# Kernel tuning notes

Hardware: AMD Instinct MI355X
Metric: run time of the kernel (lower is better)

## Reference

```python
import jax, jax.numpy as jnp
import numpy as np
from jax import lax

LOG2PI = float(np.log(2.0 * np.pi))
N_K, N_T, N_C, N_D, N_SPK = 256, 128, 32, 10, 1000000

def _std_normal_logpdf(x):
    return -0.5 * (x * x + LOG2PI)

def _normal_logpdf(x, mu, log_sig):
    z = (x - mu) * jnp.exp(-log_sig)
    return -0.5 * (z * z + LOG2PI) - log_sig

def safe_log(x, minval=1e-10):
    return jnp.log(x + minval)

def setup_inputs() -> dict:
    key = jax.random.key(0)
    ks_ = jax.random.split(key, 8)
    s = jax.random.normal(ks_[0], (N_SPK, N_D), dtype=jnp.float32)
    y = jax.random.normal(ks_[1], (N_K, N_T), dtype=jnp.float32)
    ks = jax.random.randint(ks_[2], (N_SPK,), 0, N_K, dtype=jnp.int32)
    ts = jax.random.randint(ks_[3], (N_SPK,), 0, N_T, dtype=jnp.int32)
    means = jax.random.normal(ks_[4], (N_C, N_D), dtype=jnp.float32)
    A = jax.random.normal(ks_[5], (N_C, N_D, N_D), dtype=jnp.float32)
    covs = jnp.einsum('cij,ckj->cik', A, A) / N_D + jnp.eye(N_D, dtype=jnp.float32)
    b_mu = jax.random.normal(ks_[6], (N_C,), dtype=jnp.float32)
    b_log_sig = jax.random.normal(ks_[7], (N_C,), dtype=jnp.float32)
    beta_mu = jax.random.normal(jax.random.fold_in(key, 10), (N_C, N_T), dtype=jnp.float32)
    beta_log_sig = jax.random.normal(jax.random.fold_in(key, 11), (N_C, N_T), dtype=jnp.float32)
    return {"s": s, "y": y, "ks": ks, "ts": ts, "means": means, "covs": covs,
            "b_mu": b_mu, "b_log_sig": b_log_sig, "beta_mu": beta_mu, "beta_log_sig": beta_log_sig}

def _mvn_ll(s, means, covs):
    # ll[n, c] = MVN(means[c], covs[c]).log_prob(s[n]); loop over small n_c via lax.map
    L = jnp.linalg.cholesky(covs)                       # (c, d, d)
    logdet = 2.0 * jnp.sum(jnp.log(jnp.diagonal(L, axis1=1, axis2=2)), axis=1)  # (c,)
    d = s.shape[1]
    def comp(args):
        mu, Lc, ld = args
        diff = s - mu                                   # (n, d)
        z = jax.scipy.linalg.solve_triangular(Lc, diff.T, lower=True)  # (d, n)
        return -0.5 * (d * LOG2PI + ld + jnp.sum(z * z, axis=0))       # (n,)
    return lax.map(comp, (means, L, logdet)).T          # (n, c)

def reference(s, y, ks, ts, means, covs, b_mu, b_log_sig, beta_mu, beta_log_sig):
    # sampling=False path: use variational means
    b_sample, beta_sample = b_mu, beta_mu               # (c,), (c, t)
    # log_lambdas[k, c, t] = b[c] + beta[c, t] * y[k, t]
    log_lambdas = b_sample[None, :, None] + beta_sample[None, :, :] * y[:, None, :]
    log_pis = jax.nn.log_softmax(log_lambdas, axis=1)   # (k, c, t)
    ll = _mvn_ll(s, means, covs)                        # (n, c)
    logits = ll + log_pis[ks, :, ts]                    # per-spike gather -> (n, c)
    r = jax.nn.softmax(logits, axis=1)                  # responsibilities (n, c)
    log_prior = jnp.sum(_std_normal_logpdf(b_sample)) + jnp.sum(_std_normal_logpdf(beta_sample))
    log_q = jnp.sum(_normal_logpdf(b_sample, b_mu, b_log_sig)) + \
            jnp.sum(_normal_logpdf(beta_sample, beta_mu, beta_log_sig))
    elbo = log_prior - log_q
    elbo += jnp.sum(r * logits)
    elbo -= jnp.sum(r * safe_log(r))
    return elbo
```

## Files before the change

### kernel.cpp

```cpp
#include <hip/hip_runtime.h>
#include <hip/hip_bf16.h>
#include <hip/hip_fp16.h>
#include <math.h>

#define NK 256
#define NT 128
#define NC 32
#define ND 10
#define NSPK 1000000
#define LOG2PI 1.8378770664093453f
#define NCHUNK ((NSPK + 255) / 256)
#define GRID 1024

#define FSTR 36
#define LDS_DW (256 * FSTR)

typedef __attribute__((ext_vector_type(8))) short short8;
typedef __attribute__((ext_vector_type(4))) float floatx4;
typedef __attribute__((ext_vector_type(4))) int intx4;

union FragCvt { intx4 i; short8 s; };
union H2Cvt { int i; __half2 h; };


__device__ inline unsigned pack_bf16(float a, float b) {
  __hip_bfloat16 ha = __float2bfloat16(a), hb = __float2bfloat16(b);
  unsigned short ua, ub;
  __builtin_memcpy(&ua, &ha, 2);
  __builtin_memcpy(&ub, &hb, 2);
  return (unsigned)ua | ((unsigned)ub << 16);
}

__global__ void prep_kernel(const float* __restrict__ y,
                            const float* __restrict__ means,
                            const float* __restrict__ covs,
                            const float* __restrict__ b_mu,
                            const float* __restrict__ b_ls,
                            const float* __restrict__ beta_mu,
                            const float* __restrict__ beta_ls,
                            int* __restrict__ wt,
                            float* __restrict__ cpack,
                            __half* __restrict__ pisT,
                            double* __restrict__ acc,
                            unsigned int* __restrict__ counter,
                            unsigned int* __restrict__ queue) {
  int blk = blockIdx.x;
  int tid = threadIdx.x;

  if (blk == 0) {
    int c = tid;
    if (c >= NC) return;

    float M[ND][ND];
    #pragma unroll
    for (int i = 0; i < ND; ++i)
      #pragma unroll
      for (int j = 0; j < ND; ++j)
        M[i][j] = covs[c * ND * ND + i * ND + j];

    float logdet = 0.f;
    #pragma unroll
    for (int j = 0; j < ND; ++j) {
      float d = M[j][j];
      #pragma unroll
      for (int k = 0; k < ND; ++k) if (k < j) d -= M[j][k] * M[j][k];
      float sq = sqrtf(d);
      M[j][j] = sq;
      logdet += 2.f * __logf(sq);
      float inv = 1.f / sq;
      #pragma unroll
      for (int i = 0; i < ND; ++i) {
        if (i > j) {
          float s2 = M[i][j];
          #pragma unroll
          for (int k = 0; k < ND; ++k) if (k < j) s2 -= M[i][k] * M[j][k];
          M[i][j] = s2 * inv;
        }
      }
    }

    #pragma unroll
    for (int j = 0; j < ND; ++j) {
      M[j][j] = 1.f / M[j][j];
      #pragma unroll
      for (int i = 0; i < ND; ++i) {
        if (i > j) {
          float s2 = 0.f;
          #pragma unroll
          for (int k = 0; k < ND; ++k) if (k >= j && k < i) s2 += M[i][k] * M[k][j];
          M[i][j] = -s2 / M[i][i];
        }
      }
    }

    float pd[ND];
    #pragma unroll
    for (int i = 0; i < ND; ++i) {
      #pragma unroll
      for (int jj = 0; jj < ND; ++jj) {
        if (jj >= i) {
          float s2 = 0.f;
          #pragma unroll
          for (int k = 0; k < ND; ++k) if (k >= jj) s2 += M[k][i] * M[k][jj];
          if (jj > i) M[i][jj] = s2;
          else pd[i] = s2;
        }
      }
    }

    float mu[ND], q[ND];
    #pragma unroll
    for (int i = 0; i < ND; ++i) mu[i] = means[c * ND + i];
    float muPmu = 0.f;
    #pragma unroll
    for (int i = 0; i < ND; ++i) {
      float a2 = pd[i] * mu[i];
      #pragma unroll
      for (int j = 0; j < ND; ++j) {
        if (j < i) a2 += M[j][i] * mu[j];
        if (j > i) a2 += M[i][j] * mu[j];
      }
      q[i] = a2;
      muPmu += mu[i] * a2;
    }
    float cst = -0.5f * ((float)ND * LOG2PI + logdet + muPmu);

    float wv[64];
    int p = 0;
    #pragma unroll
    for (int i = 0; i < ND; ++i)
      #pragma unroll
      for (int j = 0; j < ND; ++j)
        if (j >= i && !(i == 9 && j == 9))
          wv[p++] = (i == j) ? -0.5f * pd[i] : -M[i][j];
    #pragma unroll
    for (int i = 0; i < ND; ++i) wv[54 + i] = q[i];

    #pragma unroll
    for (int j = 0; j < 32; ++j) {
      float a = wv[2 * j], b = wv[2 * j + 1];
      float ah = __bfloat162float(__float2bfloat16(a));
      float bh = __bfloat162float(__float2bfloat16(b));
      wt[c * 32 + j] = (int)pack_bf16(ah, bh);
      wt[(32 + c) * 32 + j] = (int)pack_bf16(a - ah, b - bh);
    }
    cpack[c] = cst;
    cpack[32 + c] = -0.5f * pd[9];

  } else if (blk == 1) {
    float local = 0.f;
    for (int i = tid; i < NC; i += 256)
      local += fmaf(-0.5f * b_mu[i], b_mu[i], b_ls[i]);
    for (int i = tid; i < NC * NT; i += 256)
      local += fmaf(-0.5f * beta_mu[i], beta_mu[i], beta_ls[i]);
    #pragma unroll
    for (int off = 32; off > 0; off >>= 1) local += __shfl_down(local, off);
    __shared__ float red[4];
    if ((tid & 63) == 0) red[tid >> 6] = local;
    __syncthreads();
    if (tid == 0) {
      acc[0] = (double)(red[0] + red[1] + red[2] + red[3]);
      counter[0] = 0u;
      queue[0] = GRID;
    }

  } else {
    int id = (blk - 2) * 256 + tid;
    int t = id & (NT - 1);
    float yv = y[id];
    float v[NC];
    float m = -1e30f;
    #pragma unroll
    for (int c = 0; c < NC; ++c) {
      v[c] = fmaf(beta_mu[c * NT + t], yv, b_mu[c]);
      m = fmaxf(m, v[c]);
    }
    float ssum = 0.f;
    #pragma unroll
    for (int c = 0; c < NC; ++c) ssum += __expf(v[c] - m);
    float lz = m + __logf(ssum);
    __half* outp = pisT + (size_t)id * NC;
    #pragma unroll
    for (int c = 0; c < NC; ++c) outp[c] = __float2half(v[c] - lz);
  }
}

__global__ void __launch_bounds__(256)
__attribute__((amdgpu_waves_per_eu(4, 4)))
spike_kernel(const float* __restrict__ s,
             const int* __restrict__ ks,
             const int* __restrict__ ts,
             const int* __restrict__ wt,
             const float* __restrict__ cpack,
             const __half* __restrict__ pisT,
             double* __restrict__ acc,
             unsigned int* __restrict__ counter,
             unsigned int* __restrict__ queue,
             float* __restrict__ out) {
  __shared__ int lds[LDS_DW];
  __shared__ float red[4];
  __shared__ int nextc_sh;

  int tid = threadIdx.x;
  int wv_ = tid >> 6, L = tid & 63;
  int r = L & 15, q = L >> 4;

  FragCvt bf[2][2][2];
  #pragma unroll
  for (int h = 0; h < 2; ++h)
    #pragma unroll
    for (int nt = 0; nt < 2; ++nt)
      #pragma unroll
      for (int ks2 = 0; ks2 < 2; ++ks2)
        bf[h][nt][ks2].i =
            *(const intx4*)&wt[(h * 32 + nt * 16 + r) * 32 + ks2 * 16 + q * 4];

  float lse_sum = 0.f;

  int chunk = blockIdx.x;
  float svc[ND];
  int ktc;
  {
    int n = chunk * 256 + tid;
    int nc = n < NSPK ? n : (NSPK - 1);
    const float2* srow = (const float2*)(s + (size_t)nc * ND);
    #pragma unroll
    for (int i = 0; i < 5; ++i) {
      float2 v2 = srow[i];
      svc[2 * i] = v2.x;
      svc[2 * i + 1] = v2.y;
    }
    ktc = ks[nc] * NT + ts[nc];
  }

  while (chunk < NCHUNK) {
    int ncur = chunk * 256 + tid;

    __syncthreads();

    {
      int rb = tid * FSTR;
      float f[8];
      int p = 0;
      #pragma unroll
      for (int i = 0; i < ND; ++i) {
        #pragma unroll
        for (int j = i; j < ND; ++j) {
          if (i == 9 && j == 9) continue;
          f[p & 7] = svc[i] * svc[j];
          if ((p & 7) == 7) {
            intx4 v;
            v.x = (int)pack_bf16(f[0], f[1]);
            v.y = (int)pack_bf16(f[2], f[3]);
            v.z = (int)pack_bf16(f[4], f[5]);
            v.w = (int)pack_bf16(f[6], f[7]);
            *(intx4*)&lds[rb + (p >> 3) * 4] = v;
          }
          ++p;
        }
      }
      #pragma unroll
      for (int i = 0; i < ND; ++i) {
        f[p & 7] = svc[i];
        if ((p & 7) == 7) {
          intx4 v;
          v.x = (int)pack_bf16(f[0], f[1]);
          v.y = (int)pack_bf16(f[2], f[3]);
          v.z = (int)pack_bf16(f[4], f[5]);
          v.w = (int)pack_bf16(f[6], f[7]);
          *(intx4*)&lds[rb + (p >> 3) * 4] = v;
        }
        ++p;
      }
    }

    if (tid == 0) nextc_sh = (int)atomicAdd(queue, 1u);

    __syncthreads();

    int nextc = nextc_sh;

    float svn[ND];
    int ktn;
    {
      int cc = nextc < NCHUNK ? nextc : (NCHUNK - 1);
      int n = cc * 256 + tid;
      int nc = n < NSPK ? n : (NSPK - 1);
      const float2* srow = (const float2*)(s + (size_t)nc * ND);
      #pragma unroll
      for (int i = 0; i < 5; ++i) {
        float2 v2 = srow[i];
        svn[2 * i] = v2.x;
        svn[2 * i + 1] = v2.y;
      }
      ktn = ks[nc] * NT + ts[nc];
    }

    floatx4 accf[4][2];
    #pragma unroll
    for (int mt = 0; mt < 4; ++mt)
      #pragma unroll
      for (int nt = 0; nt < 2; ++nt)
        accf[mt][nt] = (floatx4){0.f, 0.f, 0.f, 0.f};

    #pragma unroll
    for (int mt = 0; mt < 4; ++mt) {
      #pragma unroll
      for (int ks2 = 0; ks2 < 2; ++ks2) {
        FragCvt a;
        a.i = *(const intx4*)&lds[(wv_ * 64 + mt * 16 + r) * FSTR + ks2 * 16 + q * 4];
        #pragma unroll
        for (int nt = 0; nt < 2; ++nt) {
          accf[mt][nt] = __builtin_amdgcn_mfma_f32_16x16x32_bf16(
              a.s, bf[0][nt][ks2].s, accf[mt][nt], 0, 0, 0);
          accf[mt][nt] = __builtin_amdgcn_mfma_f32_16x16x32_bf16(
              a.s, bf[1][nt][ks2].s, accf[mt][nt], 0, 0, 0);
        }
      }
    }

    __syncthreads();

    #pragma unroll
    for (int mt = 0; mt < 4; ++mt)
      #pragma unroll
      for (int nt = 0; nt < 2; ++nt)
        #pragma unroll
        for (int rr = 0; rr < 4; ++rr) {
          int srow_ = wv_ * 64 + mt * 16 + q * 4 + rr;
          lds[srow_ * FSTR + nt * 16 + r] = __float_as_int(accf[mt][nt][rr]);
        }
    __syncthreads();

    {
      const intx4* lpp = (const intx4*)(pisT + (size_t)ktc * NC);
      intx4 lraw[4];
      #pragma unroll
      for (int i = 0; i < 4; ++i) lraw[i] = lpp[i];

      float s9sq = svc[9] * svc[9];
      int base = tid * FSTR;
      float lg[32];
      #pragma unroll
      for (int g = 0; g < 8; ++g) {
        intx4 lv = *(const intx4*)&lds[base + g * 4];
        lg[4 * g + 0] = __int_as_float(lv.x);
        lg[4 * g + 1] = __int_as_float(lv.y);
        lg[4 * g + 2] = __int_as_float(lv.z);
        lg[4 * g + 3] = __int_as_float(lv.w);
      }
      #pragma unroll
      for (int g = 0; g < 16; ++g) {
        H2Cvt hc;
        hc.i = ((const int*)lraw)[g];
        float lo = __low2float(hc.h), hi = __high2float(hc.h);
        lg[2 * g + 0] += lo + fmaf(cpack[32 + 2 * g + 0], s9sq, cpack[2 * g + 0]);
        lg[2 * g + 1] += hi + fmaf(cpack[32 + 2 * g + 1], s9sq, cpack[2 * g + 1]);
      }

      float m = lg[0];
      #pragma unroll
      for (int c = 1; c < 32; ++c) m = fmaxf(m, lg[c]);
      float ssum = 0.f;
      #pragma unroll
      for (int c = 0; c < 32; ++c) ssum += __expf(lg[c] - m);
      if (ncur < NSPK) lse_sum += m + __logf(ssum);
    }

    chunk = nextc;
    ktc = ktn;
    #pragma unroll
    for (int i = 0; i < ND; ++i) svc[i] = svn[i];
  }

  #pragma unroll
  for (int off = 32; off > 0; off >>= 1) lse_sum += __shfl_down(lse_sum, off);
  if ((tid & 63) == 0) red[tid >> 6] = lse_sum;
  __syncthreads();
  if (tid == 0) {
    atomicAdd(acc, (double)(red[0] + red[1] + red[2] + red[3]));
    __threadfence();
    unsigned int old = atomicAdd(counter, 1u);
    if (old == GRID - 1) {
      __threadfence();
      double v = atomicAdd(acc, 0.0);
      out[0] = (float)v;
    }
  }
}

extern "C" void kernel_launch(void* const* d_in, const int* in_sizes, int n_in,
                              void* d_out, int out_size, void* d_ws, size_t ws_size,
                              hipStream_t stream) {
  const float* s       = (const float*)d_in[0];
  const float* y       = (const float*)d_in[1];
  const int*   ks      = (const int*)d_in[2];
  const int*   ts      = (const int*)d_in[3];
  const float* means   = (const float*)d_in[4];
  const float* covs    = (const float*)d_in[5];
  const float* b_mu    = (const float*)d_in[6];
  const float* b_ls    = (const float*)d_in[7];
  const float* beta_mu = (const float*)d_in[8];
  const float* beta_ls = (const float*)d_in[9];
  float* out = (float*)d_out;

  char* ws = (char*)d_ws;
  double* acc           = (double*)ws;
  unsigned int* counter = (unsigned int*)(ws + 8);
  unsigned int* queue   = (unsigned int*)(ws + 12);
  float* cpack          = (float*)(ws + 64);
  int* wt               = (int*)(ws + 1024);
  __half* pisT          = (__half*)(ws + 16384);

  prep_kernel<<<2 + (NK * NT) / 256, 256, 0, stream>>>(
      y, means, covs, b_mu, b_ls, beta_mu, beta_ls, wt, cpack, pisT, acc,
      counter, queue);
  spike_kernel<<<GRID, 256, 0, stream>>>(
      s, ks, ts, wt, cpack, pisT, acc, counter, queue, out);
}
```

Measured before the change: 169.0 us.

## Make spike kernel wave-independent with static scheduling and per-wave LDS

Each wave now processes its own 64-spike chunk with a private LDS slice, which removes the block-wide __syncthreads and the atomic work queue in favor of a static grid-stride over waves. The MFMA roles are swapped so the weights are the A operand and spike features the B operand, letting results be written back as float4 rows. The per-cluster constant is folded into the gathered log-pi table by a separate prep kernel, which adds a kernel launch. The pisT gather is issued earlier to hide its latency. Static scheduling can cause load imbalance, and NSPK/64 divides evenly, so no tail guard is needed.

```diff
diff --git a/kernel.cpp b/kernel.cpp
--- a/kernel.cpp
+++ b/kernel.cpp
@@ -9,11 +9,10 @@
 #define ND 10
 #define NSPK 1000000
 #define LOG2PI 1.8378770664093453f
-#define NCHUNK ((NSPK + 255) / 256)
+#define NWCHUNK (NSPK / 64)
 #define GRID 1024
-
-#define FSTR 36
-#define LDS_DW (256 * FSTR)
+#define NWAVES (GRID * 4)
+#define LSTR 33
 
 typedef __attribute__((ext_vector_type(8))) short short8;
 typedef __attribute__((ext_vector_type(4))) float floatx4;
@@ -31,19 +30,16 @@
   return (unsigned)ua | ((unsigned)ub << 16);
 }
 
-__global__ void prep_kernel(const float* __restrict__ y,
-                            const float* __restrict__ means,
-                            const float* __restrict__ covs,
-                            const float* __restrict__ b_mu,
-                            const float* __restrict__ b_ls,
-                            const float* __restrict__ beta_mu,
-                            const float* __restrict__ beta_ls,
-                            int* __restrict__ wt,
-                            float* __restrict__ cpack,
-                            __half* __restrict__ pisT,
-                            double* __restrict__ acc,
-                            unsigned int* __restrict__ counter,
-                            unsigned int* __restrict__ queue) {
+__global__ void prep1_kernel(const float* __restrict__ means,
+                             const float* __restrict__ covs,
+                             const float* __restrict__ b_mu,
+                             const float* __restrict__ b_ls,
+                             const float* __restrict__ beta_mu,
+                             const float* __restrict__ beta_ls,
+                             int* __restrict__ wt,
+                             float* __restrict__ cpack,
+                             double* __restrict__ acc,
+                             unsigned int* __restrict__ counter) {
   int blk = blockIdx.x;
   int tid = threadIdx.x;
 
@@ -108,7 +104,7 @@
       }
     }
 
-    float mu[ND], q[ND];
+    float mu[ND], qv[ND];
     #pragma unroll
     for (int i = 0; i < ND; ++i) mu[i] = means[c * ND + i];
     float muPmu = 0.f;
@@ -120,7 +116,7 @@
         if (j < i) a2 += M[j][i] * mu[j];
         if (j > i) a2 += M[i][j] * mu[j];
       }
-      q[i] = a2;
+      qv[i] = a2;
       muPmu += mu[i] * a2;
     }
     float cst = -0.5f * ((float)ND * LOG2PI + logdet + muPmu);
@@ -134,7 +130,7 @@
         if (j >= i && !(i == 9 && j == 9))
           wv[p++] = (i == j) ? -0.5f * pd[i] : -M[i][j];
     #pragma unroll
-    for (int i = 0; i < ND; ++i) wv[54 + i] = q[i];
+    for (int i = 0; i < ND; ++i) wv[54 + i] = qv[i];
 
     #pragma unroll
     for (int j = 0; j < 32; ++j) {
@@ -147,7 +143,7 @@
     cpack[c] = cst;
     cpack[32 + c] = -0.5f * pd[9];
 
-  } else if (blk == 1) {
+  } else {
     float local = 0.f;
     for (int i = tid; i < NC; i += 256)
       local += fmaf(-0.5f * b_mu[i], b_mu[i], b_ls[i]);
@@ -161,28 +157,32 @@
     if (tid == 0) {
       acc[0] = (double)(red[0] + red[1] + red[2] + red[3]);
       counter[0] = 0u;
-      queue[0] = GRID;
-    }
-
-  } else {
-    int id = (blk - 2) * 256 + tid;
-    int t = id & (NT - 1);
-    float yv = y[id];
-    float v[NC];
-    float m = -1e30f;
-    #pragma unroll
-    for (int c = 0; c < NC; ++c) {
-      v[c] = fmaf(beta_mu[c * NT + t], yv, b_mu[c]);
-      m = fmaxf(m, v[c]);
-    }
-    float ssum = 0.f;
-    #pragma unroll
-    for (int c = 0; c < NC; ++c) ssum += __expf(v[c] - m);
-    float lz = m + __logf(ssum);
-    __half* outp = pisT + (size_t)id * NC;
-    #pragma unroll
-    for (int c = 0; c < NC; ++c) outp[c] = __float2half(v[c] - lz);
+    }
   }
+}
+
+__global__ void prep2_kernel(const float* __restrict__ y,
+                             const float* __restrict__ b_mu,
+                             const float* __restrict__ beta_mu,
+                             const float* __restrict__ cpack,
+                             __half* __restrict__ pisT) {
+  int id = blockIdx.x * 256 + threadIdx.x;
+  int t = id & (NT - 1);
+  float yv = y[id];
+  float v[NC];
+  float m = -1e30f;
+  #pragma unroll
+  for (int c = 0; c < NC; ++c) {
+    v[c] = fmaf(beta_mu[c * NT + t], yv, b_mu[c]);
+    m = fmaxf(m, v[c]);
+  }
+  float ssum = 0.f;
+  #pragma unroll
+  for (int c = 0; c < NC; ++c) ssum += __expf(v[c] - m);
+  float lz = m + __logf(ssum);
+  __half* outp = pisT + (size_t)id * NC;
+  #pragma unroll
+  for (int c = 0; c < NC; ++c) outp[c] = __float2half(v[c] - lz + cpack[c]);
 }
 
 __global__ void __launch_bounds__(256)
@@ -195,51 +195,57 @@
              const __half* __restrict__ pisT,
              double* __restrict__ acc,
              unsigned int* __restrict__ counter,
-             unsigned int* __restrict__ queue,
              float* __restrict__ out) {
-  __shared__ int lds[LDS_DW];
+  __shared__ int lds[4 * 64 * LSTR];
   __shared__ float red[4];
-  __shared__ int nextc_sh;
 
   int tid = threadIdx.x;
-  int wv_ = tid >> 6, L = tid & 63;
+  int wid = tid >> 6, L = tid & 63;
   int r = L & 15, q = L >> 4;
-
-  FragCvt bf[2][2][2];
+  int* ldsw = &lds[wid * 64 * LSTR];
+
+  FragCvt wf[2][2][2];
   #pragma unroll
   for (int h = 0; h < 2; ++h)
     #pragma unroll
-    for (int nt = 0; nt < 2; ++nt)
-      #pragma unroll
-      for (int ks2 = 0; ks2 < 2; ++ks2)
-        bf[h][nt][ks2].i =
-            *(const intx4*)&wt[(h * 32 + nt * 16 + r) * 32 + ks2 * 16 + q * 4];
+    for (int mt = 0; mt < 2; ++mt)
+      #pragma unroll
+      for (int kk = 0; kk < 2; ++kk)
+        wf[h][mt][kk].i =
+            *(const intx4*)&wt[(h * 32 + mt * 16 + r) * 32 + kk * 16 + q * 4];
+
+  float w99v[NC];
+  #pragma unroll
+  for (int c = 0; c < NC; ++c) w99v[c] = cpack[32 + c];
 
   float lse_sum = 0.f;
-
-  int chunk = blockIdx.x;
+  int g = blockIdx.x * 4 + wid;
+
+  int c = g;
   float svc[ND];
-  int ktc;
+  int kvc, tvc;
   {
-    int n = chunk * 256 + tid;
-    int nc = n < NSPK ? n : (NSPK - 1);
-    const float2* srow = (const float2*)(s + (size_t)nc * ND);
+    int n = c * 64 + L;
+    const float2* srow = (const float2*)(s + (size_t)n * ND);
     #pragma unroll
     for (int i = 0; i < 5; ++i) {
       float2 v2 = srow[i];
       svc[2 * i] = v2.x;
       svc[2 * i + 1] = v2.y;
     }
-    ktc = ks[nc] * NT + ts[nc];
+    kvc = ks[n];
+    tvc = ts[n];
   }
 
-  while (chunk < NCHUNK) {
-    int ncur = chunk * 256 + tid;
-
-    __syncthreads();
+  while (c < NWCHUNK) {
+    int ktc = kvc * NT + tvc;
+    const intx4* lpp = (const intx4*)(pisT + (size_t)ktc * NC);
+    intx4 lraw[4];
+    #pragma unroll
+    for (int i = 0; i < 4; ++i) lraw[i] = lpp[i];
 
     {
-      int rb = tid * FSTR;
+      int rb = L * LSTR;
       float f[8];
       int p = 0;
       #pragma unroll
@@ -254,7 +260,7 @@
             v.y = (int)pack_bf16(f[2], f[3]);
             v.z = (int)pack_bf16(f[4], f[5]);
             v.w = (int)pack_bf16(f[6], f[7]);
-            *(intx4*)&lds[rb + (p >> 3) * 4] = v;
+            *(intx4*)&ldsw[rb + (p >> 3) * 4] = v;
           }
           ++p;
         }
@@ -268,107 +274,92 @@
           v.y = (int)pack_bf16(f[2], f[3]);
           v.z = (int)pack_bf16(f[4], f[5]);
           v.w = (int)pack_bf16(f[6], f[7]);
-          *(intx4*)&lds[rb + (p >> 3) * 4] = v;
+          *(intx4*)&ldsw[rb + (p >> 3) * 4] = v;
         }
         ++p;
       }
     }
 
-    if (tid == 0) nextc_sh = (int)atomicAdd(queue, 1u);
-
-    __syncthreads();
-
-    int nextc = nextc_sh;
-
+    int c2 = c + NWAVES;
     float svn[ND];
-    int ktn;
+    int kvn, tvn;
     {
-      int cc = nextc < NCHUNK ? nextc : (NCHUNK - 1);
-      int n = cc * 256 + tid;
-      int nc = n < NSPK ? n : (NSPK - 1);
-      const float2* srow = (const float2*)(s + (size_t)nc * ND);
+      int cc = c2 < NWCHUNK ? c2 : 0;
+      int n2 = cc * 64 + L;
+      const float2* srow = (const float2*)(s + (size_t)n2 * ND);
       #pragma unroll
       for (int i = 0; i < 5; ++i) {
         float2 v2 = srow[i];
         svn[2 * i] = v2.x;
         svn[2 * i + 1] = v2.y;
       }
-      ktn = ks[nc] * NT + ts[nc];
-    }
-
-    floatx4 accf[4][2];
-    #pragma unroll
-    for (int mt = 0; mt < 4; ++mt)
-      #pragma unroll
-      for (int nt = 0; nt < 2; ++nt)
+      kvn = ks[n2];
+      tvn = ts[n2];
+    }
+
+    floatx4 accf[2][4];
+    #pragma unroll
+    for (int mt = 0; mt < 2; ++mt)
+      #pragma unroll
+      for (int nt = 0; nt < 4; ++nt)
         accf[mt][nt] = (floatx4){0.f, 0.f, 0.f, 0.f};
 
     #pragma unroll
-    for (int mt = 0; mt < 4; ++mt) {
-      #pragma unroll
-      for (int ks2 = 0; ks2 < 2; ++ks2) {
-        FragCvt a;
-        a.i = *(const intx4*)&lds[(wv_ * 64 + mt * 16 + r) * FSTR + ks2 * 16 + q * 4];
-        #pragma unroll
-        for (int nt = 0; nt < 2; ++nt) {
-          accf[mt][nt] = __builtin_amdgcn_mfma_f32_16x16x32_bf16(
-              a.s, bf[0][nt][ks2].s, accf[mt][nt], 0, 0, 0);
-          accf[mt][nt] = __builtin_amdgcn_mfma_f32_16x16x32_bf16(
-              a.s, bf[1][nt][ks2].s, accf[mt][nt], 0, 0, 0);
-        }
-      }
-    }
-
-    __syncthreads();
-
-    #pragma unroll
-    for (int mt = 0; mt < 4; ++mt)
-      #pragma unroll
-      for (int nt = 0; nt < 2; ++nt)
-        #pragma unroll
-        for (int rr = 0; rr < 4; ++rr) {
-          int srow_ = wv_ * 64 + mt * 16 + q * 4 + rr;
-          lds[srow_ * FSTR + nt * 16 + r] = __float_as_int(accf[mt][nt][rr]);
-        }
-    __syncthreads();
+    for (int nt = 0; nt < 4; ++nt) {
+      FragCvt b0, b1;
+      b0.i = *(const intx4*)&ldsw[(nt * 16 + r) * LSTR + q * 4];
+      b1.i = *(const intx4*)&ldsw[(nt * 16 + r) * LSTR + 16 + q * 4];
+      #pragma unroll
+      for (int mt = 0; mt < 2; ++mt) {
+        accf[mt][nt] = __builtin_amdgcn_mfma_f32_16x16x32_bf16(
+            wf[0][mt][0].s, b0.s, accf[mt][nt], 0, 0, 0);
+        accf[mt][nt] = __builtin_amdgcn_mfma_f32_16x16x32_bf16(
+            wf[1][mt][0].s, b0.s, accf[mt][nt], 0, 0, 0);
+        accf[mt][nt] = __builtin_amdgcn_mfma_f32_16x16x32_bf16(
+            wf[0][mt][1].s, b1.s, accf[mt][nt], 0, 0, 0);
+        accf[mt][nt] = __builtin_amdgcn_mfma_f32_16x16x32_bf16(
+            wf[1][mt][1].s, b1.s, accf[mt][nt], 0, 0, 0);
+      }
+    }
+
+    #pragma unroll
+    for (int nt = 0; nt < 4; ++nt)
+      #pragma unroll
+      for (int mt = 0; mt < 2; ++mt)
+        *(floatx4*)&ldsw[(nt * 16 + r) * LSTR + mt * 16 + q * 4] = accf[mt][nt];
 
     {
-      const intx4* lpp = (const intx4*)(pisT + (size_t)ktc * NC);
-      intx4 lraw[4];
-      #pragma unroll
-      for (int i = 0; i < 4; ++i) lraw[i] = lpp[i];
-
+      int rb = L * LSTR;
+      float lg[NC];
+      #pragma unroll
+      for (int gch = 0; gch < 8; ++gch) {
+        intx4 lv = *(const intx4*)&ldsw[rb + gch * 4];
+        lg[4 * gch + 0] = __int_as_float(lv.x);
+        lg[4 * gch + 1] = __int_as_float(lv.y);
+        lg[4 * gch + 2] = __int_as_float(lv.z);
+        lg[4 * gch + 3] = __int_as_float(lv.w);
+      }
       float s9sq = svc[9] * svc[9];
-      int base = tid * FSTR;
-      float lg[32];
-      #pragma unroll
-      for (int g = 0; g < 8; ++g) {
-        intx4 lv = *(const intx4*)&lds[base + g * 4];
-        lg[4 * g + 0] = __int_as_float(lv.x);
-        lg[4 * g + 1] = __int_as_float(lv.y);
-        lg[4 * g + 2] = __int_as_float(lv.z);
-        lg[4 * g + 3] = __int_as_float(lv.w);
-      }
-      #pragma unroll
-      for (int g = 0; g < 16; ++g) {
+      #pragma unroll
+      for (int gg = 0; gg < 16; ++gg) {
         H2Cvt hc;
-        hc.i = ((const int*)lraw)[g];
-        float lo = __low2float(hc.h), hi = __high2float(hc.h);
-        lg[2 * g + 0] += lo + fmaf(cpack[32 + 2 * g + 0], s9sq, cpack[2 * g + 0]);
-        lg[2 * g + 1] += hi + fmaf(cpack[32 + 2 * g + 1], s9sq, cpack[2 * g + 1]);
+        hc.i = ((const int*)lraw)[gg];
+        lg[2 * gg + 0] += __low2float(hc.h) + w99v[2 * gg + 0] * s9sq;
+        lg[2 * gg + 1] += __high2float(hc.h) + w99v[2 * gg + 1] * s9sq;
       }
 
       float m = lg[0];
       #pragma unroll
-      for (int c = 1; c < 32; ++c) m = fmaxf(m, lg[c]);
+      for (int cc = 1; cc < NC; ++cc) m = fmaxf(m, lg[cc]);
       float ssum = 0.f;
       #pragma unroll
-      for (int c = 0; c < 32; ++c) ssum += __expf(lg[c] - m);
-      if (ncur < NSPK) lse_sum += m + __logf(ssum);
-    }
-
-    chunk = nextc;
-    ktc = ktn;
+      for (int cc = 0; cc < NC; ++cc) ssum += __expf(lg[cc] - m);
+      lse_sum += m + __logf(ssum);
+    }
+
+    c = c2;
+    kvc = kvn;
+    tvc = tvn;
     #pragma unroll
     for (int i = 0; i < ND; ++i) svc[i] = svn[i];
   }
@@ -407,14 +398,14 @@
   char* ws = (char*)d_ws;
   double* acc           = (double*)ws;
   unsigned int* counter = (unsigned int*)(ws + 8);
-  unsigned int* queue   = (unsigned int*)(ws + 12);
   float* cpack          = (float*)(ws + 64);
   int* wt               = (int*)(ws + 1024);
   __half* pisT          = (__half*)(ws + 16384);
 
-  prep_kernel<<<2 + (NK * NT) / 256, 256, 0, stream>>>(
-      y, means, covs, b_mu, b_ls, beta_mu, beta_ls, wt, cpack, pisT, acc,
-      counter, queue);
+  prep1_kernel<<<2, 256, 0, stream>>>(
+      means, covs, b_mu, b_ls, beta_mu, beta_ls, wt, cpack, acc, counter);
+  prep2_kernel<<<(NK * NT) / 256, 256, 0, stream>>>(
+      y, b_mu, beta_mu, cpack, pisT);
   spike_kernel<<<GRID, 256, 0, stream>>>(
-      s, ks, ts, wt, cpack, pisT, acc, counter, queue, out);
+      s, ks, ts, wt, cpack, pisT, acc, counter, out);
 }
```

New measurement: 168.8 us. About the same (-0.2%).
